# Kernel optimization log

Hardware: AMD Instinct MI355X
Metric: run time of the kernel (lower is better)

The kernel has to match this reference:

```python
import jax, jax.numpy as jnp
import numpy as np

N = 100_000      # nodes
E = 1_600_000    # edges (avg degree 16)
B = 64           # graphs in batch
OUT = 40         # out_channels (ModelNet40)
EPS = 1e-5       # BatchNorm eps


def _lin(x, W, b):
    # torch Linear: W is [out, in]
    return x @ W.T + b


def _bn_relu(y, g, be):
    # BatchNorm1d in training mode (batch statistics, biased var) + ReLU
    mean = y.mean(0)
    var = ((y - mean) ** 2).mean(0)
    return jax.nn.relu((y - mean) * jax.lax.rsqrt(var + EPS) * g + be)


def _mlp(x, layers):
    for (W, b, g, be) in layers:
        x = _bn_relu(_lin(x, W, b), g, be)
    return x


def _edge_conv(x, src, dst, layers):
    # PyG EdgeConv: message = nn(cat[x_i, x_j - x_i]), max-aggregate at target i
    xi = x[dst]                         # [E, F]
    xj = x[src]                         # [E, F]
    m = _mlp(jnp.concatenate([xi, xj - xi], axis=1), layers)  # [E, F_out]
    out = jax.ops.segment_max(m, dst, num_segments=x.shape[0])
    return jnp.where(jnp.isfinite(out), out, 0.0)  # empty segments -> 0


def setup_inputs() -> dict:
    key = jax.random.key(0)
    ks = jax.random.split(key, 16)
    d = {}
    d['pos'] = jax.random.normal(ks[0], (N, 3), dtype=jnp.float32)
    d['edge_index'] = jax.random.randint(ks[1], (2, E), 0, N, dtype=jnp.int64)
    d['batch'] = jnp.sort(jax.random.randint(ks[2], (N,), 0, B, dtype=jnp.int64))
    lin_shapes = {1: (64, 6), 2: (64, 64), 3: (64, 64), 4: (64, 128),
                  5: (128, 128), 6: (128, 128), 7: (128, 128), 8: (OUT, 128)}
    for i, (o, inp) in lin_shapes.items():
        kw = jax.random.fold_in(key, 100 + i)
        kb = jax.random.fold_in(key, 200 + i)
        s = 1.0 / np.sqrt(inp)
        d[f'W{i}'] = jax.random.uniform(kw, (o, inp), jnp.float32, -s, s)
        d[f'b{i}'] = jax.random.uniform(kb, (o,), jnp.float32, -s, s)
        if i < 8:
            d[f'g{i}'] = jnp.ones((o,), jnp.float32)
            d[f'be{i}'] = jnp.zeros((o,), jnp.float32)
    return d


def reference(pos, edge_index, batch,
              W1, b1, g1, be1, W2, b2, g2, be2, W3, b3, g3, be3,
              W4, b4, g4, be4, W5, b5, g5, be5, W6, b6, g6, be6,
              W7, b7, g7, be7, W8, b8):
    src, dst = edge_index[0], edge_index[1]
    conv1 = [(W1, b1, g1, be1), (W2, b2, g2, be2), (W3, b3, g3, be3)]
    conv2 = [(W4, b4, g4, be4)]
    x1 = _edge_conv(pos, src, dst, conv1)          # [N, 64]
    x2 = _edge_conv(x1, src, dst, conv2)           # [N, 64]
    h = _bn_relu(_lin(jnp.concatenate([x1, x2], axis=1), W5, b5), g5, be5)  # [N,128]
    pooled = jax.ops.segment_max(h, batch, num_segments=B)  # [B,128]
    pooled = jnp.where(jnp.isfinite(pooled), pooled, 0.0)
    h = _bn_relu(_lin(pooled, W6, b6), g6, be6)    # Dropout(0.5) = identity at eval
    h = _bn_relu(_lin(h, W7, b7), g7, be7)
    logits = _lin(h, W8, b8)                       # [B, OUT]
    return jax.nn.log_softmax(logits, axis=1)
```

## Files before the change

kernel.cpp:

```cpp
#include <hip/hip_runtime.h>
#include <hip/hip_bf16.h>
#include <hip/hip_fp16.h>
#include <math.h>

#define EPS_BN 1e-5f
#define NBK 256


typedef float f32x4_t  __attribute__((ext_vector_type(4)));
typedef _Float16 half8_t __attribute__((ext_vector_type(8)));
typedef _Float16 half2_t __attribute__((ext_vector_type(2)));

static __device__ __forceinline__ float bf2f(unsigned short b){
  return __uint_as_float(((unsigned)b) << 16);
}
static __device__ __forceinline__ float h2f(unsigned short u){
  _Float16 h;
  __builtin_memcpy(&h, &u, 2);
  return (float)h;
}
static __device__ __forceinline__ unsigned short f2h(float f){
  _Float16 h = (_Float16)f;
  unsigned short u;
  __builtin_memcpy(&u, &h, 2);
  return u;
}
static __device__ __forceinline__ unsigned pkh2(float a, float b){
  half2_t t = { (_Float16)a, (_Float16)b };
  unsigned u;
  __builtin_memcpy(&u, &t, 4);
  return u;
}
static inline int cdiv(int a, int b){ return (a + b - 1) / b; }
static __device__ __forceinline__ int clampi(int v, int lo, int hi){
  return v < lo ? lo : (v > hi ? hi : v);
}
static __device__ __forceinline__ int ld_idx(const void* p, long e, int m64){
  return m64 ? (int)((const long long*)p)[e] : ((const int*)p)[e];
}
static __device__ __forceinline__ unsigned ordf(float f){
  unsigned b = __float_as_uint(f);
  return (b & 0x80000000u) ? ~b : (b | 0x80000000u);
}
static __device__ __forceinline__ float iordf(unsigned u){
  unsigned b = (u & 0x80000000u) ? (u & 0x7FFFFFFFu) : ~u;
  return __uint_as_float(b);
}

__global__ void k_sentinel(float* out, int n){
  int i = blockIdx.x*256 + threadIdx.x;
  if (i < n) out[i] = -12288.0f;
}

__global__ void k_detect(const void* ei, const void* pos, int* dmode){
  __shared__ int nz, ff;
  if (threadIdx.x == 0){ nz = 0; ff = 0; }
  __syncthreads();
  const int* w32 = (const int*)ei;
  if (w32[1 + 2*threadIdx.x] != 0) nz = 1;
  const unsigned short* ph = (const unsigned short*)pos;
  int bad = 0;
  for (int i = threadIdx.x; i < 8192; i += 256)
    if (((ph[i] >> 7) & 0xFF) == 0xFF) bad = 1;
  if (bad) ff = 1;
  __syncthreads();
  if (threadIdx.x == 0){ dmode[0] = nz ? 0 : 1; dmode[1] = ff; }
}

struct ExpItem { const void* s; float* d; int n; };
struct ExpArgs { ExpItem it[31]; };
__global__ void k_expand(ExpArgs a, int cnt, const int* dmode){
  int i = blockIdx.y;
  if (i >= cnt) return;
  int m32 = dmode[1];
  int t = blockIdx.x*256 + threadIdx.x;
  if (t < a.it[i].n){
    a.it[i].d[t] = m32 ? ((const float*)a.it[i].s)[t]
                       : bf2f(((const unsigned short*)a.it[i].s)[t]);
  }
}

__global__ void k_prep(const float* __restrict__ W2, const float* __restrict__ W3,
                       const float* __restrict__ W5, const float* __restrict__ W4,
                       unsigned short* __restrict__ W2h, unsigned short* __restrict__ W3h,
                       unsigned short* __restrict__ W5h,
                       unsigned short* __restrict__ P, unsigned short* __restrict__ Q){
  int i = blockIdx.x*256 + threadIdx.x;
  if (i < 4096) W2h[i] = f2h(W2[i]);
  else if (i < 8192) W3h[i-4096] = f2h(W3[i-4096]);
  else if (i < 24576) W5h[i-8192] = f2h(W5[i-8192]);
  else if (i < 28672){
    int j = i - 24576;
    int c = j >> 6, k = j & 63;
    float b = W4[c*128 + 64 + k];
    P[j] = f2h(W4[c*128 + k] - b);
    Q[j] = f2h(b);
  }
}

__global__ void k_chist(const void* __restrict__ ei, int E, int N, const int* dmode,
                        int KK, int* __restrict__ cbc){
  __shared__ int lh[NBK];
  int tid = threadIdx.x;
  lh[tid] = 0;
  __syncthreads();
  int m64 = dmode[0];
  long base = (long)blockIdx.x*4096;
  for (int k = 0; k < 16; k++){
    long e = base + k*256 + tid;
    if (e < E){
      int nd = clampi(ld_idx(ei, (long)E + e, m64), 0, N-1);
      atomicAdd(&lh[nd/KK], 1);
    }
  }
  __syncthreads();
  if (lh[tid]) atomicAdd(&cbc[tid], lh[tid]);
}

__global__ void k_cscan(const int* __restrict__ cbc, int* __restrict__ cof,
                        int* __restrict__ cursorC){
  __shared__ int s[NBK];
  int t = threadIdx.x;
  int d = cbc[t];
  s[t] = d;
  __syncthreads();
  for (int off = 1; off < NBK; off <<= 1){
    int x = (t >= off) ? s[t - off] : 0;
    __syncthreads();
    s[t] += x;
    __syncthreads();
  }
  cof[t + 1] = s[t];
  cursorC[t] = s[t] - d;
  if (t == 0) cof[0] = 0;
}

__global__ void k_fillA(const void* __restrict__ ei, int E, int N, const int* dmode,
                        int KK, const float* __restrict__ pos,
                        int* __restrict__ cursorC, int2* __restrict__ tmp,
                        float* __restrict__ mom){
  __shared__ int lh[NBK];
  __shared__ int rb[NBK];
  int tid = threadIdx.x;
  lh[tid] = 0;
  __syncthreads();
  int m64 = dmode[0];
  long base = (long)blockIdx.x*4096;
  for (int k = 0; k < 16; k++){
    long e = base + k*256 + tid;
    if (e < E){
      int nd = clampi(ld_idx(ei, (long)E + e, m64), 0, N-1);
      atomicAdd(&lh[nd/KK], 1);
    }
  }
  __syncthreads();
  int c = lh[tid];
  rb[tid] = c ? atomicAdd(&cursorC[tid], c) : 0;
  lh[tid] = 0;
  __syncthreads();
  float v[27];
  #pragma unroll
  for (int j = 0; j < 27; j++) v[j] = 0.f;
  for (int k = 0; k < 16; k++){
    long e = base + k*256 + tid;
    if (e < E){
      int sv = clampi(ld_idx(ei, e, m64), 0, N-1);
      int nd = clampi(ld_idx(ei, (long)E + e, m64), 0, N-1);
      int b = nd/KK;
      int p = rb[b] + atomicAdd(&lh[b], 1);
      tmp[p] = make_int2(nd, sv);
      float xd0=pos[nd*3+0], xd1=pos[nd*3+1], xd2=pos[nd*3+2];
      float xs0=pos[sv*3+0], xs1=pos[sv*3+1], xs2=pos[sv*3+2];
      v[0]+=xd0; v[1]+=xd1; v[2]+=xd2;
      v[3]+=xs0; v[4]+=xs1; v[5]+=xs2;
      v[6]+=xd0*xd0; v[7]+=xd0*xd1; v[8]+=xd0*xd2; v[9]+=xd1*xd1; v[10]+=xd1*xd2; v[11]+=xd2*xd2;
      v[12]+=xs0*xs0; v[13]+=xs0*xs1; v[14]+=xs0*xs2; v[15]+=xs1*xs1; v[16]+=xs1*xs2; v[17]+=xs2*xs2;
      v[18]+=xd0*xs0; v[19]+=xd0*xs1; v[20]+=xd0*xs2;
      v[21]+=xd1*xs0; v[22]+=xd1*xs1; v[23]+=xd1*xs2;
      v[24]+=xd2*xs0; v[25]+=xd2*xs1; v[26]+=xd2*xs2;
    }
  }
  #pragma unroll
  for (int m = 1; m < 64; m <<= 1){
    #pragma unroll
    for (int j = 0; j < 27; j++) v[j] += __shfl_xor(v[j], m, 64);
  }
  int lane = tid & 63;
  int wflat = (blockIdx.x*256 + tid) >> 6;
  if (lane == 0){
    float* mr = &mom[(size_t)(wflat & 63)*32];
    #pragma unroll
    for (int j = 0; j < 27; j++) atomicAdd(&mr[j], v[j]);
  }
}

__global__ void __launch_bounds__(512, 1)
k_fillB(const int2* __restrict__ tmp, const int* __restrict__ cof, int N, int E, int KK,
        int* __restrict__ deg, int* __restrict__ offs, int2* __restrict__ es){
  __shared__ int lh[512];
  __shared__ int lc[512];
  int tid = threadIdx.x, b = blockIdx.x;
  int nd0 = b*KK;
  int nd1 = nd0 + KK; if (nd1 > N) nd1 = N;
  int nn = nd1 - nd0; if (nn < 0) nn = 0;
  int gbase = cof[b], gend = cof[b+1];
  int cnt = gend - gbase;
  lh[tid] = 0;
  __syncthreads();
  for (int t = tid; t < cnt; t += 512)
    atomicAdd(&lh[tmp[gbase + t].x - nd0], 1);
  __syncthreads();
  int d = lh[tid];
  for (int off = 1; off < 512; off <<= 1){
    int x = (tid >= off) ? lh[tid - off] : 0;
    __syncthreads();
    lh[tid] += x;
    __syncthreads();
  }
  int excl = lh[tid] - d;
  if (tid < nn){
    deg[nd0 + tid] = d;
    offs[nd0 + tid] = gbase + excl;
  }
  lc[tid] = excl;
  if (b == gridDim.x - 1 && tid == 0) offs[N] = E;
  __syncthreads();
  for (int t = tid; t < cnt; t += 512){
    int2 e2 = tmp[gbase + t];
    int lpos = atomicAdd(&lc[e2.x - nd0], 1);
    es[gbase + lpos] = e2;
  }
}

__global__ void k_bn1(const float* __restrict__ mom, float Ef,
                      const float* __restrict__ W1, const float* __restrict__ b1,
                      const float* __restrict__ g, const float* __restrict__ be,
                      float* __restrict__ ss){
  __shared__ float sm[27];
  int t = threadIdx.x;
  if (t < 27){
    float s = 0.f;
    for (int r = 0; r < 64; r++) s += mom[(size_t)r*32 + t];
    sm[t] = s;
  }
  __syncthreads();
  if (t < 64){
    float P0 = W1[t*6+0]-W1[t*6+3], P1 = W1[t*6+1]-W1[t*6+4], P2 = W1[t*6+2]-W1[t*6+5];
    float Q0 = W1[t*6+3], Q1 = W1[t*6+4], Q2 = W1[t*6+5];
    float b = b1[t];
    float vD0=sm[0],vD1=sm[1],vD2=sm[2], vS0=sm[3],vS1=sm[4],vS2=sm[5];
    float PvD = P0*vD0 + P1*vD1 + P2*vD2;
    float QvS = Q0*vS0 + Q1*vS1 + Q2*vS2;
    float sum = PvD + QvS + Ef*b;
    float PMDP = P0*(sm[6]*P0 + sm[7]*P1 + sm[8]*P2)
               + P1*(sm[7]*P0 + sm[9]*P1 + sm[10]*P2)
               + P2*(sm[8]*P0 + sm[10]*P1 + sm[11]*P2);
    float QMSQ = Q0*(sm[12]*Q0 + sm[13]*Q1 + sm[14]*Q2)
               + Q1*(sm[13]*Q0 + sm[15]*Q1 + sm[16]*Q2)
               + Q2*(sm[14]*Q0 + sm[16]*Q1 + sm[17]*Q2);
    float PGQ = P0*(sm[18]*Q0 + sm[19]*Q1 + sm[20]*Q2)
              + P1*(sm[21]*Q0 + sm[22]*Q1 + sm[23]*Q2)
              + P2*(sm[24]*Q0 + sm[25]*Q1 + sm[26]*Q2);
    float sumsq = PMDP + 2.f*b*PvD + Ef*b*b + QMSQ + 2.f*(PGQ + b*QvS);
    float mean = sum / Ef;
    float var  = fmaxf(sumsq / Ef - mean*mean, 0.f);
    float inv  = rsqrtf(var + EPS_BN);
    float sc   = g[t] * inv;
    ss[t]      = sc;
    ss[64 + t] = be[t] - mean*sc;
  }
}

__global__ void k_ab(const float* __restrict__ pos, int N,
                     const float* __restrict__ W1, const float* __restrict__ b1,
                     const float* __restrict__ ss1,
                     unsigned short* __restrict__ at, unsigned short* __restrict__ bt){
  int n = blockIdx.x*256 + threadIdx.x;
  if (n >= N) return;
  float x0 = pos[n*3+0], x1 = pos[n*3+1], x2 = pos[n*3+2];
  unsigned short* ar = at + (size_t)n*64;
  unsigned short* br = bt + (size_t)n*64;
  #pragma unroll
  for (int c2 = 0; c2 < 64; c2 += 2){
    float av[2], bv[2];
    #pragma unroll
    for (int u = 0; u < 2; u++){
      int c = c2 + u;
      float q0 = W1[c*6+3], q1 = W1[c*6+4], q2 = W1[c*6+5];
      float p0 = W1[c*6+0]-q0, p1 = W1[c*6+1]-q1, p2 = W1[c*6+2]-q2;
      float sc = ss1[c], sh = ss1[64+c];
      float pa = fmaf(p0,x0, fmaf(p1,x1, fmaf(p2,x2, b1[c])));
      float qb = fmaf(q0,x0, fmaf(q1,x1, q2*x2));
      av[u] = fmaf(pa, sc, sh);
      bv[u] = qb * sc;
    }
    *(unsigned*)&ar[c2] = pkh2(av[0], av[1]);
    *(unsigned*)&br[c2] = pkh2(bv[0], bv[1]);
  }
}

__global__ void k_finalize(float* __restrict__ repl, int C, float count,
                           const float* __restrict__ g, const float* __restrict__ be,
                           float* __restrict__ ss){
  int c = threadIdx.x;
  if (c < C){
    float s = 0.f, q = 0.f;
    for (int r = 0; r < 64; r++){
      s += repl[r*256 + c];       repl[r*256 + c] = 0.f;
      q += repl[r*256 + 128 + c]; repl[r*256 + 128 + c] = 0.f;
    }
    float mean = s / count;
    float var  = fmaxf(q / count - mean*mean, 0.f);
    float inv  = rsqrtf(var + EPS_BN);
    float sc   = g[c] * inv;
    ss[c]     = sc;
    ss[C + c] = be[c] - mean*sc;
  }
}

template<int NT, int KT>
static __device__ __forceinline__ void loadBh2(const unsigned short* __restrict__ Wp, int c15, int q,
                                               half8_t bf[NT][KT]){
  #pragma unroll
  for (int nt = 0; nt < NT; nt++){
    int c = nt*16 + c15;
    #pragma unroll
    for (int kt = 0; kt < KT; kt++)
      bf[nt][kt] = *(const half8_t*)(Wp + (size_t)c*(KT*32) + kt*32 + q*8);
  }
}
template<int NT, int KT, int ST>
static __device__ __forceinline__ void do_mfma2(const unsigned short* Aw, half8_t bf[NT][KT],
                                                const float* __restrict__ bias, int c15, int q,
                                                f32x4_t acc[4][NT]){
  #pragma unroll
  for (int mt = 0; mt < 4; mt++)
    #pragma unroll
    for (int nt = 0; nt < NT; nt++){
      float bv = bias[nt*16 + c15];
      acc[mt][nt] = (f32x4_t){bv, bv, bv, bv};
    }
  #pragma unroll
  for (int mt = 0; mt < 4; mt++){
    #pragma unroll
    for (int kt = 0; kt < KT; kt++){
      half8_t af = *(const half8_t*)&Aw[(mt*16 + c15)*ST + kt*32 + q*8];
      #pragma unroll
      for (int nt = 0; nt < NT; nt++)
        acc[mt][nt] = __builtin_amdgcn_mfma_f32_16x16x32_f16(af, bf[nt][kt], acc[mt][nt], 0, 0, 0);
    }
  }
}
template<int NT>
static __device__ __forceinline__ void stats_acc2(f32x4_t acc[4][NT], long tb, int E,
                                                  int lane, int q, int r_idx, int choff,
                                                  float* __restrict__ repl){
  #pragma unroll
  for (int nt = 0; nt < NT; nt++){
    float s = 0.f, qq = 0.f;
    #pragma unroll
    for (int mt = 0; mt < 4; mt++){
      #pragma unroll
      for (int r = 0; r < 4; r++){
        long eidx = tb + mt*16 + q*4 + r;
        float v = (eidx < E) ? acc[mt][nt][r] : 0.f;
        s += v; qq += v*v;
      }
    }
    s += __shfl_xor(s, 16, 64); qq += __shfl_xor(qq, 16, 64);
    s += __shfl_xor(s, 32, 64); qq += __shfl_xor(qq, 32, 64);
    if (lane < 16){
      atomicAdd(&repl[r_idx*256 + choff + nt*16 + lane], s);
      atomicAdd(&repl[r_idx*256 + 128 + choff + nt*16 + lane], qq);
    }
  }
}
template<int NT, int ST>
static __device__ __forceinline__ void dumpC2(f32x4_t acc[4][NT], unsigned short* Cw,
                                              int colbase, int c15, int q){
  #pragma unroll
  for (int mt = 0; mt < 4; mt++)
    #pragma unroll
    for (int nt = 0; nt < NT; nt++){
      int col = colbase + nt*16 + c15;
      #pragma unroll
      for (int r = 0; r < 4; r += 2){
        unsigned p = pkh2(acc[mt][nt][r], acc[mt][nt][r+1]);
        int row = mt*16 + q*4 + r;
        Cw[row*ST + col]        = (unsigned short)p;
        Cw[(row + 1)*ST + col]  = (unsigned short)(p >> 16);
      }
    }
}
static __device__ __forceinline__ void dumpC2T(f32x4_t acc[4][2], unsigned short* CT,
                                               int colbase, int c15, int q){
  #pragma unroll
  for (int mt = 0; mt < 4; mt++)
    #pragma unroll
    for (int nt = 0; nt < 2; nt++){
      int col = colbase + nt*16 + c15;
      #pragma unroll
      for (int r = 0; r < 4; r += 2){
        unsigned p = pkh2(acc[mt][nt][r], acc[mt][nt][r+1]);
        int row = mt*16 + q*4 + r;
        *(unsigned*)((char*)CT + col*136 + row*2) = p;
      }
    }
}
static __device__ __forceinline__ void seg_walk3(const unsigned short* CT, const int* nds,
                                                 long tb, int E, int tid,
                                                 unsigned* __restrict__ tmax,
                                                 unsigned* __restrict__ tmin){
  int lane = tid & 63, par = tid >> 6;
  long rem = (long)E - tb;
  int limit = rem >= 64 ? 64 : (rem > 0 ? (int)rem : 0);
  int k0 = par*32;
  int cnt = limit - k0; if (cnt > 32) cnt = 32;
  if (cnt <= 0) return;
  const char* base = (const char*)CT + lane*136 + k0*2;
  uint2 dv[8];
  #pragma unroll
  for (int j = 0; j < 8; j++) dv[j] = *(const uint2*)(base + j*8);
  int nd[32];
  #pragma unroll
  for (int j = 0; j < 8; j++) *(int4*)&nd[j*4] = *(const int4*)&nds[k0 + j*4];
  int cur = nd[0];
  float mx = -3.4e38f, mn = 3.4e38f;
  #pragma unroll
  for (int k = 0; k < 32; k++){
    unsigned w = (k & 2) ? dv[k>>2].y : dv[k>>2].x;
    unsigned short hv = (k & 1) ? (unsigned short)(w >> 16) : (unsigned short)(w & 0xffffu);
    float v = h2f(hv);
    bool act = (k < cnt);
    int ndk = act ? nd[k] : cur;
    if (ndk != cur){
      atomicMax(&tmax[(size_t)cur*64 + lane], ordf(mx));
      atomicMin(&tmin[(size_t)cur*64 + lane], ordf(mn));
      cur = ndk; mx = v; mn = v;
    } else if (act){
      mx = fmaxf(mx, v); mn = fminf(mn, v);
    }
  }
  atomicMax(&tmax[(size_t)cur*64 + lane], ordf(mx));
  atomicMin(&tmin[(size_t)cur*64 + lane], ordf(mn));
}
static __device__ __forceinline__ unsigned rladd2h(unsigned a, unsigned b){
  half2_t ha, hb;
  __builtin_memcpy(&ha, &a, 4);
  __builtin_memcpy(&hb, &b, 4);
  half2_t s = ha + hb;
  half2_t z = { (_Float16)0, (_Float16)0 };
  half2_t r = __builtin_elementwise_max(s, z);
  unsigned u;
  __builtin_memcpy(&u, &r, 4);
  return u;
}
static __device__ __forceinline__ void stage_z1t_half(const unsigned short* __restrict__ at,
                                                      const unsigned short* __restrict__ bt,
                                                      int di, int si, int h, unsigned short* Ar){
  const uint4* a4 = (const uint4*)(at + (size_t)di*64 + h*32);
  const uint4* b4 = (const uint4*)(bt + (size_t)si*64 + h*32);
  #pragma unroll
  for (int k = 0; k < 4; k++){
    uint4 av = a4[k], bv = b4[k], o;
    o.x = rladd2h(av.x, bv.x); o.y = rladd2h(av.y, bv.y);
    o.z = rladd2h(av.z, bv.z); o.w = rladd2h(av.w, bv.w);
    *(uint4*)&Ar[k*8] = o;
  }
}

__global__ void __launch_bounds__(128, 1)
k_m2stats(const int2* __restrict__ es,
          const unsigned short* __restrict__ at, const unsigned short* __restrict__ bt,
          int E,
          const unsigned short* __restrict__ W2h, const float* __restrict__ b2,
          float* __restrict__ repl){
  __shared__ unsigned short A[64][72];
  int tid = threadIdx.x;
  int lane = tid & 63, wv = tid >> 6;
  long tb = (long)blockIdx.x*64;
  long e = tb + lane;
  unsigned short* Ar = &A[lane][wv*32];
  if (e < E){
    int2 e2 = es[e];
    stage_z1t_half(at, bt, e2.x, e2.y, wv, Ar);
  } else {
    #pragma unroll
    for (int k = 0; k < 4; k++) *(uint4*)&Ar[k*8] = make_uint4(0u,0u,0u,0u);
  }
  __syncthreads();
  int c15 = lane & 15, q = lane >> 4;
  half8_t bf[2][2];
  loadBh2<2,2>(W2h + (size_t)(wv*32)*64, c15, q, bf);
  f32x4_t acc[4][2];
  do_mfma2<2,2,72>(&A[0][0], bf, b2 + wv*32, c15, q, acc);
  stats_acc2<2>(acc, tb, E, lane, q, blockIdx.x & 63, wv*32, repl);
}

__global__ void __launch_bounds__(128, 1)
k_conv1f(const unsigned short* __restrict__ at, const unsigned short* __restrict__ bt,
         const int2* __restrict__ es, int E,
         const float* __restrict__ ss2,
         const unsigned short* __restrict__ W2h, const float* __restrict__ b2,
         const unsigned short* __restrict__ W3h, const float* __restrict__ b3,
         float* __restrict__ repl, unsigned* __restrict__ tmax, unsigned* __restrict__ tmin){
  __shared__ unsigned short A[64][72];
  __shared__ int nds[64];
  int tid = threadIdx.x;
  int lane = tid & 63, wv = tid >> 6;
  long tb = (long)blockIdx.x*64;
  long t = tb + lane;
  unsigned short* Ar = &A[lane][wv*32];
  if (t < E){
    int2 e2 = es[t];
    if (wv == 0) nds[lane] = e2.x;
    stage_z1t_half(at, bt, e2.x, e2.y, wv, Ar);
  } else {
    if (wv == 0) nds[lane] = 0;
    #pragma unroll
    for (int k = 0; k < 4; k++) *(uint4*)&Ar[k*8] = make_uint4(0u,0u,0u,0u);
  }
  __syncthreads();
  int c15 = lane & 15, q = lane >> 4;
  unsigned short* Aw = &A[0][0];
  f32x4_t acc[4][2];
  {
    half8_t bf[2][2];
    loadBh2<2,2>(W2h + (size_t)(wv*32)*64, c15, q, bf);
    do_mfma2<2,2,72>(Aw, bf, b2 + wv*32, c15, q, acc);
  }
  #pragma unroll
  for (int nt = 0; nt < 2; nt++){
    int ch = wv*32 + nt*16 + c15;
    float sc = ss2[ch], sh = ss2[64 + ch];
    #pragma unroll
    for (int mt = 0; mt < 4; mt++)
      #pragma unroll
      for (int r = 0; r < 4; r++)
        acc[mt][nt][r] = fmaxf(fmaf(acc[mt][nt][r], sc, sh), 0.f);
  }
  __syncthreads();
  dumpC2<2,72>(acc, Aw, wv*32, c15, q);
  __syncthreads();
  {
    half8_t bf[2][2];
    loadBh2<2,2>(W3h + (size_t)(wv*32)*64, c15, q, bf);
    do_mfma2<2,2,72>(Aw, bf, b3 + wv*32, c15, q, acc);
  }
  stats_acc2<2>(acc, tb, E, lane, q, blockIdx.x & 63, wv*32, repl);
  __syncthreads();
  dumpC2T(acc, Aw, wv*32, c15, q);
  __syncthreads();
  seg_walk3(Aw, nds, tb, E, tid, tmax, tmin);
}

__global__ void __launch_bounds__(64, 1)
k_pq(const unsigned short* __restrict__ x1, int N,
     const unsigned short* __restrict__ Pmh, const unsigned short* __restrict__ Qmh,
     const float* __restrict__ b4, const float* __restrict__ zeros64,
     unsigned short* __restrict__ up, unsigned short* __restrict__ uq){
  __shared__ unsigned short A[64][72];
  __shared__ unsigned short Cb[64][72];
  int lane = threadIdx.x;
  long nb0 = (long)blockIdx.x*64;
  long n = nb0 + lane;
  unsigned short* Ar = &A[lane][0];
  if (n < N){
    const uint4* a4 = (const uint4*)(x1 + (size_t)n*64);
    #pragma unroll
    for (int k = 0; k < 8; k++) *(uint4*)&Ar[k*8] = a4[k];
  } else {
    #pragma unroll
    for (int k = 0; k < 8; k++) *(uint4*)&Ar[k*8] = make_uint4(0u,0u,0u,0u);
  }
  __syncthreads();
  int c15 = lane & 15, q = lane >> 4;
  unsigned short* Aw = &A[0][0];
  unsigned short* Cw = &Cb[0][0];
  for (int h = 0; h < 2; h++){
    const unsigned short* Wp = h ? Qmh : Pmh;
    const float* bp = h ? zeros64 : b4;
    unsigned short* out = h ? uq : up;
    half8_t bf[4][2];
    loadBh2<4,2>(Wp, c15, q, bf);
    f32x4_t acc[4][4];
    do_mfma2<4,2,72>(Aw, bf, bp, c15, q, acc);
    dumpC2<4,72>(acc, Cw, 0, c15, q);
    __syncthreads();
    int rl = lane >> 3, ch8 = lane & 7;
    #pragma unroll
    for (int pass = 0; pass < 8; pass++){
      int row = pass*8 + rl;
      long nn = nb0 + row;
      if (nn < N)
        *(uint4*)(out + (size_t)nn*64 + ch8*8) = *(const uint4*)&Cw[row*72 + ch8*8];
    }
    __syncthreads();
  }
}

#define NPW 8
__global__ void k_edge2(const int* __restrict__ offs, const int2* __restrict__ es,
                        const unsigned short* __restrict__ uq, const unsigned short* __restrict__ up,
                        int N, float* __restrict__ tmaxF, float* __restrict__ tminF,
                        float* __restrict__ repl){
  int wv = threadIdx.x >> 6, lane = threadIdx.x & 63;
  int w_id = blockIdx.x*4 + wv;
  int n0 = w_id * NPW;
  int nend = n0 + NPW; if (nend > N) nend = N;
  float s_acc = 0.f, ss_acc = 0.f;
  for (int n = n0; n < nend; n++){
    int e0 = offs[n], e1 = offs[n+1];
    if (e1 <= e0) continue;
    float mx = -3.4e38f, mn = 3.4e38f, qs = 0.f, qsq = 0.f;
    int t = e0;
    for (; t + 4 <= e1; t += 4){
      int s0 = es[t].y, s1 = es[t+1].y, s2 = es[t+2].y, s3 = es[t+3].y;
      float v0 = h2f(uq[(size_t)s0*64 + lane]);
      float v1 = h2f(uq[(size_t)s1*64 + lane]);
      float v2 = h2f(uq[(size_t)s2*64 + lane]);
      float v3 = h2f(uq[(size_t)s3*64 + lane]);
      mx = fmaxf(mx, fmaxf(fmaxf(v0, v1), fmaxf(v2, v3)));
      mn = fminf(mn, fminf(fminf(v0, v1), fminf(v2, v3)));
      qs += (v0 + v1) + (v2 + v3);
      qsq += v0*v0 + v1*v1 + v2*v2 + v3*v3;
    }
    for (; t < e1; t++){
      int s0 = es[t].y;
      float v0 = h2f(uq[(size_t)s0*64 + lane]);
      mx = fmaxf(mx, v0); mn = fminf(mn, v0); qs += v0; qsq += v0*v0;
    }
    float pv = h2f(up[(size_t)n*64 + lane]);
    float deg = (float)(e1 - e0);
    s_acc  += fmaf(deg, pv, qs);
    ss_acc += fmaf(deg*pv, pv, fmaf(2.f*pv, qs, qsq));
    tmaxF[(size_t)n*64 + lane] = mx;
    tminF[(size_t)n*64 + lane] = mn;
  }
  int r_idx = w_id & 63;
  atomicAdd(&repl[r_idx*256 + lane], s_acc);
  atomicAdd(&repl[r_idx*256 + 128 + lane], ss_acc);
}

__global__ void k_applybn2(unsigned short* __restrict__ x2 ,
                           const float* __restrict__ tmaxF, const float* __restrict__ tminF,
                           const int* __restrict__ degD, const float* __restrict__ ss,
                           long total){
  long i = (long)blockIdx.x*256 + threadIdx.x;
  if (i >= total) return;
  int c = (int)(i & 63);
  long n = i >> 6;
  float out = 0.f;
  if (degD[n] > 0){
    float sc = ss[c], sh = ss[64 + c];
    float v = h2f(x2[i]) + ((sc >= 0.f) ? tmaxF[i] : tminF[i]);
    out = fmaxf(fmaf(v, sc, sh), 0.f);
  }
  x2[i] = f2h(out);
}

__global__ void k_applybn(const unsigned* __restrict__ tmax, const unsigned* __restrict__ tmin,
                          const float* __restrict__ ss, long total,
                          unsigned short* __restrict__ xout){
  long i = (long)blockIdx.x*256 + threadIdx.x;
  if (i >= total) return;
  int c = (int)(i & 63);
  unsigned um = tmax[i];
  float out = 0.f;
  if (um != 0u){
    float sc = ss[c], sh = ss[64 + c];
    float v = (sc >= 0.f) ? iordf(um) : iordf(tmin[i]);
    out = fmaxf(fmaf(v, sc, sh), 0.f);
  }
  xout[i] = f2h(out);
}

__global__ void __launch_bounds__(64, 1)
k_lin5m(const unsigned short* __restrict__ x1, const unsigned short* __restrict__ x2,
        int N, const unsigned short* __restrict__ W5h, const float* __restrict__ b5,
        unsigned short* __restrict__ y5, float* __restrict__ repl){
  __shared__ unsigned short A[64][136];
  __shared__ unsigned short Cb[64][72];
  int lane = threadIdx.x;
  long nb0 = (long)blockIdx.x*64;
  long n = nb0 + lane;
  unsigned short* Ar = &A[lane][0];
  if (n < N){
    const uint4* a4 = (const uint4*)(x1 + (size_t)n*64);
    const uint4* b4 = (const uint4*)(x2 + (size_t)n*64);
    #pragma unroll
    for (int k = 0; k < 8; k++) *(uint4*)&Ar[k*8]      = a4[k];
    #pragma unroll
    for (int k = 0; k < 8; k++) *(uint4*)&Ar[64 + k*8] = b4[k];
  } else {
    #pragma unroll
    for (int k = 0; k < 16; k++) *(uint4*)&Ar[k*8] = make_uint4(0u,0u,0u,0u);
  }
  __syncthreads();
  int c15 = lane & 15, q = lane >> 4;
  int r_idx = blockIdx.x & 63;
  unsigned short* Aw = &A[0][0];
  unsigned short* Cw = &Cb[0][0];
  for (int h = 0; h < 2; h++){
    const unsigned short* Wp = W5h + (size_t)h*64*128;
    half8_t bf[4][4];
    loadBh2<4,4>(Wp, c15, q, bf);
    f32x4_t acc[4][4];
    do_mfma2<4,4,136>(Aw, bf, b5 + h*64, c15, q, acc);
    stats_acc2<4>(acc, nb0, N, lane, q, r_idx, h*64, repl);
    dumpC2<4,72>(acc, Cw, 0, c15, q);
    __syncthreads();
    int rl = lane >> 3, ch8 = lane & 7;
    #pragma unroll
    for (int pass = 0; pass < 8; pass++){
      int row = pass*8 + rl;
      long nn = nb0 + row;
      if (nn < N)
        *(uint4*)(y5 + (size_t)nn*128 + h*64 + ch8*8) = *(const uint4*)&Cw[row*72 + ch8*8];
    }
    __syncthreads();
  }
}

__global__ void k_pool(const unsigned short* __restrict__ y5, const void* __restrict__ batch, int N,
                       const int* dmode, const float* __restrict__ ss5, unsigned int* __restrict__ pooled){
  int m64 = dmode[0];
  int c = threadIdx.x & 127;
  int par = threadIdx.x >> 7;
  int n0 = blockIdx.x*128;
  int n1 = min(n0 + 128, N);
  float sc = ss5[c], sh = ss5[128 + c];
  int curb = -1; float curm = 0.f;
  for (int n = n0 + par; n < n1; n += 2){
    int b = clampi(ld_idx(batch, (long)n, m64), 0, 63);
    float v = fmaf(h2f(y5[(size_t)n*128 + c]), sc, sh);
    if (b != curb){
      if (curb >= 0) atomicMax(&pooled[curb*128 + c], __float_as_uint(fmaxf(curm, 0.f)));
      curb = b; curm = v;
    } else {
      curm = fmaxf(curm, v);
    }
  }
  if (curb >= 0) atomicMax(&pooled[curb*128 + c], __float_as_uint(fmaxf(curm, 0.f)));
}

__global__ void __launch_bounds__(1024, 1)
k_head(const unsigned int* __restrict__ pooled,
       const float* __restrict__ W6, const float* __restrict__ b6,
       const float* __restrict__ g6, const float* __restrict__ be6,
       const float* __restrict__ W7, const float* __restrict__ b7,
       const float* __restrict__ g7, const float* __restrict__ be7,
       const float* __restrict__ W8, const float* __restrict__ b8,
       float* __restrict__ out){
  __shared__ float X[64*128];
  __shared__ float Y[64*128];
  __shared__ float Z[64*40];
  __shared__ float ss[256];
  int tid = threadIdx.x;
  for (int i = tid; i < 8192; i += 1024) X[i] = __uint_as_float(pooled[i]);
  __syncthreads();
  for (int cell = tid; cell < 8192; cell += 1024){
    int r = cell >> 7, c = cell & 127;
    const float* xr = &X[r*128];
    const float* wr = &W6[c*128];
    float a = b6[c];
    for (int j = 0; j < 128; j++) a = fmaf(xr[j], wr[j], a);
    Y[cell] = a;
  }
  __syncthreads();
  if (tid < 128){
    float s = 0.f;
    for (int r = 0; r < 64; r++) s += Y[r*128 + tid];
    float mean = s * (1.f/64.f);
    float qq = 0.f;
    for (int r = 0; r < 64; r++){ float d = Y[r*128 + tid] - mean; qq += d*d; }
    float var = fmaxf(qq * (1.f/64.f), 0.f);
    float inv = rsqrtf(var + EPS_BN);
    float sc = g6[tid] * inv;
    ss[tid] = sc;
    ss[128 + tid] = be6[tid] - mean*sc;
  }
  __syncthreads();
  for (int cell = tid; cell < 8192; cell += 1024){
    int c = cell & 127;
    X[cell] = fmaxf(fmaf(Y[cell], ss[c], ss[128 + c]), 0.f);
  }
  __syncthreads();
  for (int cell = tid; cell < 8192; cell += 1024){
    int r = cell >> 7, c = cell & 127;
    const float* xr = &X[r*128];
    const float* wr = &W7[c*128];
    float a = b7[c];
    for (int j = 0; j < 128; j++) a = fmaf(xr[j], wr[j], a);
    Y[cell] = a;
  }
  __syncthreads();
  if (tid < 128){
    float s = 0.f;
    for (int r = 0; r < 64; r++) s += Y[r*128 + tid];
    float mean = s * (1.f/64.f);
    float qq = 0.f;
    for (int r = 0; r < 64; r++){ float d = Y[r*128 + tid] - mean; qq += d*d; }
    float var = fmaxf(qq * (1.f/64.f), 0.f);
    float inv = rsqrtf(var + EPS_BN);
    float sc = g7[tid] * inv;
    ss[tid] = sc;
    ss[128 + tid] = be7[tid] - mean*sc;
  }
  __syncthreads();
  for (int cell = tid; cell < 8192; cell += 1024){
    int c = cell & 127;
    X[cell] = fmaxf(fmaf(Y[cell], ss[c], ss[128 + c]), 0.f);
  }
  __syncthreads();
  for (int cell = tid; cell < 2560; cell += 1024){
    int r = cell / 40, c = cell - r*40;
    const float* xr = &X[r*128];
    const float* wr = &W8[c*128];
    float a = b8[c];
    for (int j = 0; j < 128; j++) a = fmaf(xr[j], wr[j], a);
    Z[cell] = a;
  }
  __syncthreads();
  if (tid < 64){
    const float* zr = &Z[tid*40];
    float m = zr[0];
    for (int c = 1; c < 40; c++) m = fmaxf(m, zr[c]);
    float s = 0.f;
    for (int c = 0; c < 40; c++) s += expf(zr[c] - m);
    float ls = logf(s);
    for (int c = 0; c < 40; c++) out[tid*40 + c] = zr[c] - m - ls;
  }
}

extern "C" void kernel_launch(void* const* d_in, const int* in_sizes, int n_in,
                              void* d_out, int out_size, void* d_ws, size_t ws_size,
                              hipStream_t stream) {
  const void* pos   = d_in[0];
  const void* ei    = d_in[1];
  const void* batch = d_in[2];
  (void)n_in;

  const int N = in_sizes[0] / 3;
  const int E = in_sizes[1] / 2;
  const int KK = cdiv(N, NBK);

  auto al = [](size_t x){ return (x + 255) & ~(size_t)255; };
  char* w = (char*)d_ws;
  size_t o = 0;
  float* repl = (float*)(w + o);                 o += (size_t)64*256*4;
  unsigned int* pooled = (unsigned int*)(w + o); o += (size_t)64*128*4;
  float* zeros64 = (float*)(w + o);              o += 256;
  float* mom = (float*)(w + o);                  o += (size_t)64*32*4;
  int* cbc = (int*)(w + o);                      o += 1024;
  size_t zero_bytes = o;
  int* cof = (int*)(w + o);                      o += 2048;
  int* cursorC = (int*)(w + o);                  o += 1024;
  int* deg = (int*)(w + o);                      o += al((size_t)4*N);
  unsigned* tmaxA = (unsigned*)(w + o);          o += (size_t)64*N*4;
  unsigned* tminA = (unsigned*)(w + o);          o += (size_t)64*N*4;
  float* tmaxF = (float*)tmaxA;
  float* tminF = (float*)tminA;
  int* dmode = (int*)(w + o);                    o += 256;
  int* offs = (int*)(w + o);                     o += al((size_t)4*(N + 1));
  int2* tmp = (int2*)(w + o);                    o += al((size_t)8*E);
  int2* es = (int2*)(w + o);                     o += al((size_t)8*E);
  float* ss1 = (float*)(w + o);                  o += 1024;
  float* ss2 = (float*)(w + o);                  o += 1024;
  float* ss3 = (float*)(w + o);                  o += 1024;
  float* ss4 = (float*)(w + o);                  o += 1024;
  float* ss5 = (float*)(w + o);                  o += 1024;
  unsigned short* W2h = (unsigned short*)(w + o); o += 8192;
  unsigned short* W3h = (unsigned short*)(w + o); o += 8192;
  unsigned short* W5h = (unsigned short*)(w + o); o += 32768;
  unsigned short* Pmh = (unsigned short*)(w + o); o += 8192;
  unsigned short* Qmh = (unsigned short*)(w + o); o += 8192;
  float* expBase = (float*)(w + o);
  float* ep = expBase;
  float* epos = ep; ep += (size_t)3*N;
  float* eW[9], *eb[9], *eg[9], *ebe[9];
  const int wsz[9] = {0, 64*6, 64*64, 64*64, 64*128, 128*128, 128*128, 128*128, 40*128};
  const int bsz[9] = {0, 64, 64, 64, 64, 128, 128, 128, 40};
  for (int i = 1; i <= 8; i++){
    eW[i] = ep; ep += wsz[i];
    eb[i] = ep; ep += bsz[i];
    if (i < 8){ eg[i] = ep; ep += bsz[i]; ebe[i] = ep; ep += bsz[i]; }
  }
  long expCount = (long)(ep - expBase);
  o += al((size_t)expCount * 4);
  unsigned short* x1b = (unsigned short*)(w + o); o += al((size_t)2*64*N);
  unsigned short* x2b = (unsigned short*)(w + o); o += al((size_t)2*64*N);
  unsigned short* uqb = (unsigned short*)(w + o); o += al((size_t)2*64*N);
  unsigned short* atb = (unsigned short*)(w + o); o += al((size_t)2*64*N);
  unsigned short* btb = (unsigned short*)(w + o); o += al((size_t)2*64*N);
  unsigned short* y5b = (unsigned short*)(w + o); o += al((size_t)2*128*N);

  float* out_f = (float*)d_out;
  if (ws_size < o){
    k_sentinel<<<cdiv(out_size,256), 256, 0, stream>>>(out_f, out_size);
    return;
  }

  hipMemsetAsync(w, 0, zero_bytes, stream);
  hipMemsetAsync(tmaxA, 0x00, (size_t)64*N*4, stream);
  hipMemsetAsync(tminA, 0xFF, (size_t)64*N*4, stream);
  k_detect<<<1, 256, 0, stream>>>(ei, pos, dmode);

  ExpArgs ea;
  int it = 0;
  ea.it[it++] = {pos, epos, 3*N};
  int di_idx = 3;
  for (int i = 1; i <= 8; i++){
    ea.it[it++] = {d_in[di_idx++], eW[i], wsz[i]};
    ea.it[it++] = {d_in[di_idx++], eb[i], bsz[i]};
    if (i < 8){
      ea.it[it++] = {d_in[di_idx++], eg[i], bsz[i]};
      ea.it[it++] = {d_in[di_idx++], ebe[i], bsz[i]};
    }
  }
  k_expand<<<dim3(cdiv(3*N,256), 31), 256, 0, stream>>>(ea, it, dmode);
  k_prep<<<112, 256, 0, stream>>>(eW[2], eW[3], eW[5], eW[4], W2h, W3h, W5h, Pmh, Qmh);

  const int nfb = cdiv(E, 4096);
  k_chist<<<nfb, 256, 0, stream>>>(ei, E, N, dmode, KK, cbc);
  k_cscan<<<1, 256, 0, stream>>>(cbc, cof, cursorC);
  k_fillA<<<nfb, 256, 0, stream>>>(ei, E, N, dmode, KK, epos, cursorC, tmp, mom);
  k_fillB<<<NBK, 512, 0, stream>>>(tmp, cof, N, E, KK, deg, offs, es);
  k_bn1<<<1, 64, 0, stream>>>(mom, (float)E, eW[1], eb[1], eg[1], ebe[1], ss1);
  k_ab<<<cdiv(N,256), 256, 0, stream>>>(epos, N, eW[1], eb[1], ss1, atb, btb);

  k_m2stats<<<cdiv(E,64), 128, 0, stream>>>(es, atb, btb, E, W2h, eb[2], repl);
  k_finalize<<<1, 128, 0, stream>>>(repl, 64, (float)E, eg[2], ebe[2], ss2);
  k_conv1f<<<cdiv(E,64), 128, 0, stream>>>(atb, btb, es, E, ss2,
                                           W2h, eb[2], W3h, eb[3], repl, tmaxA, tminA);
  k_finalize<<<1, 128, 0, stream>>>(repl, 64, (float)E, eg[3], ebe[3], ss3);
  k_applybn<<<cdiv(N*64,256), 256, 0, stream>>>(tmaxA, tminA, ss3, (long)N*64, x1b);

  k_pq<<<cdiv(N,64), 64, 0, stream>>>(x1b, N, Pmh, Qmh, eb[4], zeros64, x2b, uqb);
  k_edge2<<<cdiv(N, 4*NPW), 256, 0, stream>>>(offs, es, uqb, x2b, N, tmaxF, tminF, repl);
  k_finalize<<<1, 128, 0, stream>>>(repl, 64, (float)E, eg[4], ebe[4], ss4);
  k_applybn2<<<cdiv(N*64,256), 256, 0, stream>>>(x2b, tmaxF, tminF, deg, ss4, (long)N*64);

  k_lin5m<<<cdiv(N,64), 64, 0, stream>>>(x1b, x2b, N, W5h, eb[5], y5b, repl);
  k_finalize<<<1, 128, 0, stream>>>(repl, 128, (float)N, eg[5], ebe[5], ss5);
  k_pool<<<cdiv(N,128), 256, 0, stream>>>(y5b, batch, N, dmode, ss5, pooled);

  k_head<<<1, 1024, 0, stream>>>(pooled, eW[6], eb[6], eg[6], ebe[6],
                                 eW[7], eb[7], eg[7], ebe[7], eW[8], eb[8], out_f);
}
```

Before: 696.0 us.

## Split single-block MLP head into multi-block kernels

Replaces the single 1024-thread head kernel, which ran three dense layers, two batch-norms and log-softmax serially on one CU, with six small kernels. The matmuls now spread over 32 or 10 blocks, and BN+ReLU is folded into the next layer's input load. The aim is to stop the head from being bottlenecked on one compute unit. In exchange it adds five kernel launches and round-trips intermediates through global memory, where the old version kept them in shared memory.

```diff
diff --git a/kernel.cpp b/kernel.cpp
--- a/kernel.cpp
+++ b/kernel.cpp
@@ -744,93 +744,60 @@
   if (curb >= 0) atomicMax(&pooled[curb*128 + c], __float_as_uint(fmaxf(curm, 0.f)));
 }
 
-__global__ void __launch_bounds__(1024, 1)
-k_head(const unsigned int* __restrict__ pooled,
-       const float* __restrict__ W6, const float* __restrict__ b6,
-       const float* __restrict__ g6, const float* __restrict__ be6,
-       const float* __restrict__ W7, const float* __restrict__ b7,
-       const float* __restrict__ g7, const float* __restrict__ be7,
-       const float* __restrict__ W8, const float* __restrict__ b8,
-       float* __restrict__ out){
-  __shared__ float X[64*128];
-  __shared__ float Y[64*128];
-  __shared__ float Z[64*40];
-  __shared__ float ss[256];
-  int tid = threadIdx.x;
-  for (int i = tid; i < 8192; i += 1024) X[i] = __uint_as_float(pooled[i]);
-  __syncthreads();
-  for (int cell = tid; cell < 8192; cell += 1024){
-    int r = cell >> 7, c = cell & 127;
-    const float* xr = &X[r*128];
-    const float* wr = &W6[c*128];
-    float a = b6[c];
-    for (int j = 0; j < 128; j++) a = fmaf(xr[j], wr[j], a);
-    Y[cell] = a;
-  }
-  __syncthreads();
-  if (tid < 128){
-    float s = 0.f;
-    for (int r = 0; r < 64; r++) s += Y[r*128 + tid];
-    float mean = s * (1.f/64.f);
-    float qq = 0.f;
-    for (int r = 0; r < 64; r++){ float d = Y[r*128 + tid] - mean; qq += d*d; }
-    float var = fmaxf(qq * (1.f/64.f), 0.f);
-    float inv = rsqrtf(var + EPS_BN);
-    float sc = g6[tid] * inv;
-    ss[tid] = sc;
-    ss[128 + tid] = be6[tid] - mean*sc;
-  }
-  __syncthreads();
-  for (int cell = tid; cell < 8192; cell += 1024){
-    int c = cell & 127;
-    X[cell] = fmaxf(fmaf(Y[cell], ss[c], ss[128 + c]), 0.f);
-  }
-  __syncthreads();
-  for (int cell = tid; cell < 8192; cell += 1024){
-    int r = cell >> 7, c = cell & 127;
-    const float* xr = &X[r*128];
-    const float* wr = &W7[c*128];
-    float a = b7[c];
-    for (int j = 0; j < 128; j++) a = fmaf(xr[j], wr[j], a);
-    Y[cell] = a;
-  }
-  __syncthreads();
-  if (tid < 128){
-    float s = 0.f;
-    for (int r = 0; r < 64; r++) s += Y[r*128 + tid];
-    float mean = s * (1.f/64.f);
-    float qq = 0.f;
-    for (int r = 0; r < 64; r++){ float d = Y[r*128 + tid] - mean; qq += d*d; }
-    float var = fmaxf(qq * (1.f/64.f), 0.f);
-    float inv = rsqrtf(var + EPS_BN);
-    float sc = g7[tid] * inv;
-    ss[tid] = sc;
-    ss[128 + tid] = be7[tid] - mean*sc;
-  }
-  __syncthreads();
-  for (int cell = tid; cell < 8192; cell += 1024){
-    int c = cell & 127;
-    X[cell] = fmaxf(fmaf(Y[cell], ss[c], ss[128 + c]), 0.f);
-  }
-  __syncthreads();
-  for (int cell = tid; cell < 2560; cell += 1024){
-    int r = cell / 40, c = cell - r*40;
-    const float* xr = &X[r*128];
-    const float* wr = &W8[c*128];
-    float a = b8[c];
-    for (int j = 0; j < 128; j++) a = fmaf(xr[j], wr[j], a);
-    Z[cell] = a;
-  }
-  __syncthreads();
-  if (tid < 64){
-    const float* zr = &Z[tid*40];
-    float m = zr[0];
-    for (int c = 1; c < 40; c++) m = fmaxf(m, zr[c]);
-    float s = 0.f;
-    for (int c = 0; c < 40; c++) s += expf(zr[c] - m);
-    float ls = logf(s);
-    for (int c = 0; c < 40; c++) out[tid*40 + c] = zr[c] - m - ls;
-  }
+__global__ void k_linH6(const unsigned int* __restrict__ X, const float* __restrict__ W,
+                        const float* __restrict__ b, float* __restrict__ Y){
+  int cell = blockIdx.x*256 + threadIdx.x;
+  if (cell >= 8192) return;
+  int r = cell >> 7, c = cell & 127;
+  const unsigned int* xr = X + r*128;
+  const float* wr = W + c*128;
+  float a = b[c];
+  for (int j = 0; j < 128; j++) a = fmaf(__uint_as_float(xr[j]), wr[j], a);
+  Y[cell] = a;
+}
+
+__global__ void k_bnH(const float* __restrict__ Y, int CO,
+                      const float* __restrict__ g, const float* __restrict__ be,
+                      float* __restrict__ ss){
+  int c = threadIdx.x;
+  if (c >= CO) return;
+  float s = 0.f;
+  for (int r = 0; r < 64; r++) s += Y[r*CO + c];
+  float mean = s * (1.f/64.f);
+  float q = 0.f;
+  for (int r = 0; r < 64; r++){ float d = Y[r*CO + c] - mean; q += d*d; }
+  float var = fmaxf(q * (1.f/64.f), 0.f);
+  float inv = rsqrtf(var + EPS_BN);
+  float sc = g[c] * inv;
+  ss[c] = sc;
+  ss[CO + c] = be[c] - mean*sc;
+}
+
+__global__ void k_linHR(const float* __restrict__ Y, const float* __restrict__ ssH,
+                        const float* __restrict__ W, const float* __restrict__ b,
+                        int CO, float* __restrict__ Z){
+  int cell = blockIdx.x*256 + threadIdx.x;
+  if (cell >= 64*CO) return;
+  int r = cell / CO, c = cell - r*CO;
+  const float* xr = Y + r*128;
+  const float* wr = W + c*128;
+  float a = b[c];
+  for (int j = 0; j < 128; j++){
+    float x = fmaxf(fmaf(xr[j], ssH[j], ssH[128 + j]), 0.f);
+    a = fmaf(x, wr[j], a);
+  }
+  Z[cell] = a;
+}
+
+__global__ void k_logsm(const float* __restrict__ Z, float* __restrict__ out){
+  int r = threadIdx.x;
+  const float* zr = Z + r*40;
+  float m = zr[0];
+  for (int c = 1; c < 40; c++) m = fmaxf(m, zr[c]);
+  float s = 0.f;
+  for (int c = 0; c < 40; c++) s += expf(zr[c] - m);
+  float ls = logf(s);
+  for (int c = 0; c < 40; c++) out[r*40 + c] = zr[c] - m - ls;
 }
 
 extern "C" void kernel_launch(void* const* d_in, const int* in_sizes, int n_in,
@@ -870,6 +837,10 @@
   float* ss3 = (float*)(w + o);                  o += 1024;
   float* ss4 = (float*)(w + o);                  o += 1024;
   float* ss5 = (float*)(w + o);                  o += 1024;
+  float* ssH = (float*)(w + o);                  o += 1024;
+  float* Y6 = (float*)(w + o);                   o += (size_t)8192*4;
+  float* Y7 = (float*)(w + o);                   o += (size_t)8192*4;
+  float* Zl = (float*)(w + o);                   o += al((size_t)2560*4);
   unsigned short* W2h = (unsigned short*)(w + o); o += 8192;
   unsigned short* W3h = (unsigned short*)(w + o); o += 8192;
   unsigned short* W5h = (unsigned short*)(w + o); o += 32768;
@@ -945,6 +916,10 @@
   k_finalize<<<1, 128, 0, stream>>>(repl, 128, (float)N, eg[5], ebe[5], ss5);
   k_pool<<<cdiv(N,128), 256, 0, stream>>>(y5b, batch, N, dmode, ss5, pooled);
 
-  k_head<<<1, 1024, 0, stream>>>(pooled, eW[6], eb[6], eg[6], ebe[6],
-                                 eW[7], eb[7], eg[7], ebe[7], eW[8], eb[8], out_f);
-}
+  k_linH6<<<32, 256, 0, stream>>>(pooled, eW[6], eb[6], Y6);
+  k_bnH<<<1, 128, 0, stream>>>(Y6, 128, eg[6], ebe[6], ssH);
+  k_linHR<<<32, 256, 0, stream>>>(Y6, ssH, eW[7], eb[7], 128, Y7);
+  k_bnH<<<1, 128, 0, stream>>>(Y7, 128, eg[7], ebe[7], ssH);
+  k_linHR<<<10, 256, 0, stream>>>(Y7, ssH, eW[8], eb[8], 40, Zl);
+  k_logsm<<<1, 64, 0, stream>>>(Zl, out_f);
+}
```

Result: faster. 632.0 us (-9.2%).
